# Performance work log

Hardware: AMD Instinct MI355X
Metric: run time of the kernel (lower is better)

The kernel has to match this reference:

```python
import jax, jax.numpy as jnp
import numpy as np
import math

EPS = 1e-5
MAX_NORM = 1.0 - 1e-3
C = 1.0
NUM_HEADS = 8


def _project(x, c=C):
    norm = jnp.maximum(jnp.linalg.norm(x, axis=-1, keepdims=True), EPS)
    max_norm = MAX_NORM / math.sqrt(c)
    return jnp.where(norm > max_norm, x / norm * max_norm, x)


def _expmap0(v, c=C):
    sc = math.sqrt(c)
    n = jnp.maximum(jnp.linalg.norm(v, axis=-1, keepdims=True), EPS)
    return _project(jnp.tanh(sc * n) * v / (sc * n), c)


def _logmap0(y, c=C):
    sc = math.sqrt(c)
    n = jnp.maximum(jnp.linalg.norm(y, axis=-1, keepdims=True), EPS)
    return jnp.arctanh(jnp.minimum(sc * n, 1.0 - EPS)) * y / (sc * n)


def _mobius_add(x, y, c=C):
    x2 = jnp.sum(x * x, axis=-1, keepdims=True)
    y2 = jnp.sum(y * y, axis=-1, keepdims=True)
    xy = jnp.sum(x * y, axis=-1, keepdims=True)
    num = (1.0 + 2.0 * c * xy + c * y2) * x + (1.0 - c * x2) * y
    den = jnp.maximum(1.0 + 2.0 * c * xy + c * c * x2 * y2, EPS)
    return _project(num / den, c)


def _pairwise_dist(x, y, c=C):
    # x: (B,H,Q,d), y: (B,H,K,d) -> (B,H,Q,K)
    m = _mobius_add(-x[:, :, :, None, :], y[:, :, None, :, :], c)  # (B,H,Q,K,d)
    n = jnp.clip(jnp.linalg.norm(m, axis=-1), EPS, 1.0 - EPS)
    sc = math.sqrt(c)
    return (2.0 / sc) * jnp.arctanh(sc * n)


def setup_inputs() -> dict:
    key = jax.random.key(0)
    ks = jax.random.split(key, 12)
    B, S, D = 2, 512, 512
    # points on the Poincare ball via expmap0
    q = _expmap0(0.5 * jax.random.normal(ks[0], (B, S, D), jnp.float32))
    k = _expmap0(0.5 * jax.random.normal(ks[1], (B, S, D), jnp.float32))
    v = _expmap0(0.5 * jax.random.normal(ks[2], (B, S, D), jnp.float32))
    w = 0.02
    return {
        'query': q, 'key': k, 'value': v,
        'Wq': w * jax.random.normal(ks[3], (D, D), jnp.float32),
        'bq': w * jax.random.normal(ks[4], (D,), jnp.float32),
        'Wk': w * jax.random.normal(ks[5], (D, D), jnp.float32),
        'bk': w * jax.random.normal(ks[6], (D,), jnp.float32),
        'Wv': w * jax.random.normal(ks[7], (D, D), jnp.float32),
        'bv': w * jax.random.normal(ks[8], (D,), jnp.float32),
        'Wo': w * jax.random.normal(ks[9], (D, D), jnp.float32),
        'bo': w * jax.random.normal(ks[10], (D,), jnp.float32),
    }


def reference(query, key, value, Wq, bq, Wk, bk, Wv, bv, Wo, bo):
    B, Q, D = query.shape
    K = key.shape[1]
    H = NUM_HEADS
    dh = D // H
    q_tan = _logmap0(query)
    k_tan = _logmap0(key)
    v_tan = _logmap0(value)
    q = (q_tan @ Wq.T + bq).reshape(B, Q, H, dh).transpose(0, 2, 1, 3)  # (B,H,Q,dh)
    k = (k_tan @ Wk.T + bk).reshape(B, K, H, dh).transpose(0, 2, 1, 3)
    v = (v_tan @ Wv.T + bv).reshape(B, K, H, dh).transpose(0, 2, 1, 3)
    q_hyp = _expmap0(q)
    k_hyp = _expmap0(k)
    scores = -_pairwise_dist(q_hyp, k_hyp) / math.sqrt(dh)  # (B,H,Q,K)
    attn = jax.nn.softmax(scores, axis=-1)  # dropout is identity in eval
    out = jnp.einsum('bhqk,bhkd->bhqd', attn, v)
    out = out.transpose(0, 2, 1, 3).reshape(B, Q, D)
    return _expmap0(out @ Wo.T + bo)
```

## Files before the change

### kernel.cpp

```cpp
#include <hip/hip_runtime.h>
#include <cmath>

#define DEV static __device__ __forceinline__

namespace {

constexpr int B = 2, S = 512, D = 512, H = 8;
constexpr int BS = B * S;
constexpr float EPSF = 1e-5f;
constexpr float MAXN = 1.0f - 1e-3f;

typedef unsigned short u16;
typedef unsigned int u32;
typedef __attribute__((ext_vector_type(8))) short bf8_t;
typedef __attribute__((ext_vector_type(8))) _Float16 h8_t;
typedef __attribute__((ext_vector_type(4))) float f4_t;

DEV float waveSum(float v) {
#pragma unroll
  for (int o = 32; o > 0; o >>= 1) v += __shfl_xor(v, o, 64);
  return v;
}
DEV u16 f2bf(float f) {
  u32 x = __float_as_uint(f);
  u32 r = x + 0x7fffu + ((x >> 16) & 1u);
  return (u16)(r >> 16);
}
DEV float bf2f(u16 u) { return __uint_as_float(((u32)u) << 16); }
DEV u16 f2h(float f) {
  _Float16 h = (_Float16)f;
  u16 u;
  __builtin_memcpy(&u, &h, 2);
  return u;
}
DEV float tanh_pos(float n) {
  float e = __builtin_amdgcn_exp2f(2.8853900817779268f * n);
  return (e - 1.f) / (e + 1.f);
}
DEV bf8_t conv8(float4 a, float4 b) {
  bf8_t o;
  o[0] = (short)f2bf(a.x); o[1] = (short)f2bf(a.y);
  o[2] = (short)f2bf(a.z); o[3] = (short)f2bf(a.w);
  o[4] = (short)f2bf(b.x); o[5] = (short)f2bf(b.y);
  o[6] = (short)f2bf(b.z); o[7] = (short)f2bf(b.w);
  return o;
}
DEV float dot4(float4 a) { return a.x * a.x + a.y * a.y + a.z * a.z + a.w * a.w; }

__global__ __launch_bounds__(256) void gemm_qkv_f2(
    const float* __restrict__ q, const float* __restrict__ k,
    const float* __restrict__ v, const float* __restrict__ Wq,
    const float* __restrict__ Wk, const float* __restrict__ Wv,
    const float* __restrict__ bq, const float* __restrict__ bk,
    const float* __restrict__ bv, u16* __restrict__ hq, u16* __restrict__ hk,
    u16* __restrict__ vT, float* __restrict__ qn2, float* __restrict__ kn2) {
  const int z = blockIdx.z;
  const float* A = z == 0 ? q : (z == 1 ? k : v);
  const float* W = z == 0 ? Wq : (z == 1 ? Wk : Wv);
  const float* bias = z == 0 ? bq : (z == 1 ? bk : bv);
  const int i0 = blockIdx.y * 64, j0 = blockIdx.x * 64, h = blockIdx.x;
  __shared__ __align__(16) u16 As[4096], Bs[4096];
  __shared__ float facs[64];
  const int tid = threadIdx.x;
  const int w = tid >> 6, l = tid & 63, lg = l >> 4, lr = l & 15;
  const int srow = tid >> 3, scb = tid & 7;
  f4_t acc[4] = {{0, 0, 0, 0}, {0, 0, 0, 0}, {0, 0, 0, 0}, {0, 0, 0, 0}};
  float n2a = 0.f, n2b = 0.f;
  for (int kt = 0; kt < D; kt += 64) {
    const float* ap0 = A + (size_t)(i0 + srow) * D + kt + scb * 8;
    const float* ap1 = ap0 + (size_t)32 * D;
    const float* wp0 = W + (size_t)(j0 + srow) * D + kt + scb * 8;
    const float* wp1 = wp0 + (size_t)32 * D;
    float4 a00 = *(const float4*)ap0, a01 = *(const float4*)(ap0 + 4);
    float4 a10 = *(const float4*)ap1, a11 = *(const float4*)(ap1 + 4);
    float4 w00 = *(const float4*)wp0, w01 = *(const float4*)(wp0 + 4);
    float4 w10 = *(const float4*)wp1, w11 = *(const float4*)(wp1 + 4);
    n2a += dot4(a00) + dot4(a01);
    n2b += dot4(a10) + dot4(a11);
    __syncthreads();
    const int sw = 8 * (scb ^ (srow & 7));
    *(bf8_t*)&As[srow * 64 + sw] = conv8(a00, a01);
    *(bf8_t*)&As[(srow + 32) * 64 + sw] = conv8(a10, a11);
    *(bf8_t*)&Bs[srow * 64 + sw] = conv8(w00, w01);
    *(bf8_t*)&Bs[(srow + 32) * 64 + sw] = conv8(w10, w11);
    __syncthreads();
#pragma unroll
    for (int ks = 0; ks < 2; ++ks) {
      const int arow = w * 16 + lr;
      bf8_t af = *(const bf8_t*)&As[arow * 64 + 8 * ((ks * 4 + lg) ^ (arow & 7))];
#pragma unroll
      for (int nf = 0; nf < 4; ++nf) {
        const int brow = nf * 16 + lr;
        bf8_t bfr = *(const bf8_t*)&Bs[brow * 64 + 8 * ((ks * 4 + lg) ^ (brow & 7))];
        acc[nf] = __builtin_amdgcn_mfma_f32_16x16x32_bf16(af, bfr, acc[nf], 0, 0, 0);
      }
    }
  }
  n2a += __shfl_xor(n2a, 1, 64); n2a += __shfl_xor(n2a, 2, 64);
  n2a += __shfl_xor(n2a, 4, 64);
  n2b += __shfl_xor(n2b, 1, 64); n2b += __shfl_xor(n2b, 2, 64);
  n2b += __shfl_xor(n2b, 4, 64);
  if (scb == 0) {
    float na = fmaxf(sqrtf(n2a), EPSF), za = fminf(na, 1.0f - EPSF);
    facs[srow] = 0.34657359027997264f *
                 __builtin_amdgcn_logf((1.0f + za) / (1.0f - za)) / na;
    float nb = fmaxf(sqrtf(n2b), EPSF), zb = fminf(nb, 1.0f - EPSF);
    facs[srow + 32] = 0.34657359027997264f *
                      __builtin_amdgcn_logf((1.0f + zb) / (1.0f - zb)) / nb;
  }
  __syncthreads();
  float c[4][4];
#pragma unroll
  for (int nf = 0; nf < 4; ++nf) {
    const float bb = bias[j0 + nf * 16 + lr];
#pragma unroll
    for (int r = 0; r < 4; ++r)
      c[nf][r] = acc[nf][r] * facs[w * 16 + lg * 4 + r] + bb;
  }
  if (z < 2) {
    float part[4] = {0, 0, 0, 0};
#pragma unroll
    for (int nf = 0; nf < 4; ++nf)
#pragma unroll
      for (int r = 0; r < 4; ++r) part[r] += c[nf][r] * c[nf][r];
#pragma unroll
    for (int off = 1; off < 16; off <<= 1)
#pragma unroll
      for (int r = 0; r < 4; ++r) part[r] += __shfl_xor(part[r], off, 64);
    float fac[4];
#pragma unroll
    for (int r = 0; r < 4; ++r) {
      float n = fmaxf(sqrtf(part[r]), EPSF);
      fac[r] = fminf(tanh_pos(n), MAXN) / n;
    }
    u16 yb[4][4];
    float p2[4] = {0, 0, 0, 0};
#pragma unroll
    for (int nf = 0; nf < 4; ++nf)
#pragma unroll
      for (int r = 0; r < 4; ++r) {
        u16 t = f2bf(c[nf][r] * fac[r]);
        yb[nf][r] = t;
        float yf = bf2f(t);
        p2[r] += yf * yf;
      }
#pragma unroll
    for (int off = 1; off < 16; off <<= 1)
#pragma unroll
      for (int r = 0; r < 4; ++r) p2[r] += __shfl_xor(p2[r], off, 64);
    u16* dst = z == 0 ? hq : hk;
    float* n2o = z == 0 ? qn2 : kn2;
#pragma unroll
    for (int nf = 0; nf < 4; ++nf)
#pragma unroll
      for (int r = 0; r < 4; ++r)
        dst[(size_t)(i0 + w * 16 + lg * 4 + r) * D + j0 + nf * 16 + lr] = yb[nf][r];
    if (lr == 0)
#pragma unroll
      for (int r = 0; r < 4; ++r)
        n2o[h * BS + i0 + w * 16 + lg * 4 + r] = p2[r];
  } else {
    __syncthreads();
#pragma unroll
    for (int nf = 0; nf < 4; ++nf)
#pragma unroll
      for (int r = 0; r < 4; ++r) {
        const int prow = w * 16 + lg * 4 + r;
        const int pcol = nf * 16 + lr;
        As[prow * 64 + 8 * ((pcol >> 3) ^ (prow & 7)) + (pcol & 7)] = f2h(c[nf][r]);
      }
    __syncthreads();
    const int d = tid >> 2, s0 = (tid & 3) * 16;
    const int b = i0 >> 9, sb = (i0 & 511) + s0;
    bf8_t o0, o1;
#pragma unroll
    for (int j = 0; j < 8; ++j) {
      const int s = s0 + j;
      o0[j] = (short)As[s * 64 + 8 * ((d >> 3) ^ (s & 7)) + (d & 7)];
    }
#pragma unroll
    for (int j = 0; j < 8; ++j) {
      const int s = s0 + 8 + j;
      o1[j] = (short)As[s * 64 + 8 * ((d >> 3) ^ (s & 7)) + (d & 7)];
    }
    u16* dst = vT + ((size_t)((b * 8 + h) * 64 + d)) * S + sb;
    *(bf8_t*)dst = o0;
    *(bf8_t*)(dst + 8) = o1;
  }
}

__global__ __launch_bounds__(256) void fused_attn_blk(
    const u16* __restrict__ hq, const u16* __restrict__ hk,
    const u16* __restrict__ vT, const float* __restrict__ qn2,
    const float* __restrict__ kn2, u16* __restrict__ ctx) {
  const int bh = blockIdx.y, b = bh >> 3, h = bh & 7;
  const int i0 = blockIdx.x * 16;
  __shared__ __align__(16) u16 Ps[4][2][1024];
  __shared__ float rsL[4][16];
  const int tid = threadIdx.x;
  const int w = tid >> 6, l = tid & 63, lg = l >> 4, lr = l & 15;
  const int sp = w;
  bf8_t qf[2];
#pragma unroll
  for (int ks = 0; ks < 2; ++ks)
    qf[ks] = *(const bf8_t*)(hq + (size_t)(b * S + i0 + lr) * D + h * 64 +
                             ks * 32 + lg * 8);
  float qq[4];
#pragma unroll
  for (int r = 0; r < 4; ++r) qq[r] = qn2[h * BS + b * S + i0 + lg * 4 + r];
  f4_t acc_o[4] = {{0, 0, 0, 0}, {0, 0, 0, 0}, {0, 0, 0, 0}, {0, 0, 0, 0}};
  float rloc[4] = {0, 0, 0, 0};
#pragma unroll
  for (int t = 0; t < 2; ++t) {
    const int kt = sp * 2 + t;
    const int kb = b * S + kt * 64;
    bf8_t kf[2][4], vf[2][4];
#pragma unroll
    for (int ks = 0; ks < 2; ++ks)
#pragma unroll
      for (int nf = 0; nf < 4; ++nf) {
        kf[ks][nf] = *(const bf8_t*)(hk + (size_t)(kb + nf * 16 + lr) * D +
                                     h * 64 + ks * 32 + lg * 8);
        vf[ks][nf] = *(const bf8_t*)(vT + (size_t)(bh * 64 + nf * 16 + lr) * S +
                                     kt * 64 + ks * 32 + lg * 8);
      }
    float kn[4];
#pragma unroll
    for (int nf = 0; nf < 4; ++nf) kn[nf] = kn2[h * BS + kb + nf * 16 + lr];
    f4_t sa[4] = {{0, 0, 0, 0}, {0, 0, 0, 0}, {0, 0, 0, 0}, {0, 0, 0, 0}};
#pragma unroll
    for (int ks = 0; ks < 2; ++ks)
#pragma unroll
      for (int nf = 0; nf < 4; ++nf)
        sa[nf] = __builtin_amdgcn_mfma_f32_16x16x32_bf16(qf[ks], kf[ks][nf],
                                                         sa[nf], 0, 0, 0);
    u16* Pb = Ps[w][t & 1];
    float ps[4] = {0, 0, 0, 0};
#pragma unroll
    for (int nf = 0; nf < 4; ++nf) {
      const float kk = kn[nf];
#pragma unroll
      for (int r = 0; r < 4; ++r) {
        const float tt = sa[nf][r];
        float num = fmaxf(qq[r] - 2.f * tt + kk, 0.f);
        float den = fmaxf(1.f - 2.f * tt + qq[r] * kk, EPSF);
        float rr = fminf(fmaxf(sqrtf(num / den), EPSF), MAXN);
        float p = __builtin_amdgcn_exp2f(
            0.125f * __builtin_amdgcn_logf((1.f - rr) / (1.f + rr)));
        ps[r] += p;
        const int prow = lg * 4 + r, pcol = nf * 16 + lr;
        Pb[prow * 64 + 8 * ((pcol >> 3) ^ (prow & 7)) + (pcol & 7)] = f2h(p);
      }
    }
#pragma unroll
    for (int off = 1; off < 16; off <<= 1)
#pragma unroll
      for (int r = 0; r < 4; ++r) ps[r] += __shfl_xor(ps[r], off, 64);
#pragma unroll
    for (int r = 0; r < 4; ++r) rloc[r] += ps[r];
#pragma unroll
    for (int ks = 0; ks < 2; ++ks) {
      h8_t pa = *(const h8_t*)&Pb[lr * 64 + 8 * ((ks * 4 + lg) ^ (lr & 7))];
#pragma unroll
      for (int nf = 0; nf < 4; ++nf)
        acc_o[nf] = __builtin_amdgcn_mfma_f32_16x16x32_f16(pa, vf[ks][nf],
                                                           acc_o[nf], 0, 0, 0);
    }
  }
  float* myO = (float*)Ps + w * 1024;
#pragma unroll
  for (int nf = 0; nf < 4; ++nf)
#pragma unroll
    for (int r = 0; r < 4; ++r)
      myO[(lg * 4 + r) * 64 + nf * 16 + lr] = acc_o[nf][r];
  if (lr == 0)
#pragma unroll
    for (int r = 0; r < 4; ++r) rsL[w][lg * 4 + r] = rloc[r];
  __syncthreads();
  const float* OsL = (const float*)Ps;
  const int row = tid >> 4, c4 = (tid & 15) * 4;
  const float rt = rsL[0][row] + rsL[1][row] + rsL[2][row] + rsL[3][row];
  const float inv = 1.f / rt;
  f4_t s = {0, 0, 0, 0};
#pragma unroll
  for (int sp2 = 0; sp2 < 4; ++sp2)
    s += *(const f4_t*)&OsL[sp2 * 1024 + row * 64 + c4];
  ushort4 o;
  o.x = f2bf(s[0] * inv); o.y = f2bf(s[1] * inv);
  o.z = f2bf(s[2] * inv); o.w = f2bf(s[3] * inv);
  *(ushort4*)&ctx[(size_t)(b * S + i0 + row) * D + h * 64 + c4] = o;
}

__global__ __launch_bounds__(256) void gemm_out_f(
    const u16* __restrict__ A, const float* __restrict__ Wo,
    const float* __restrict__ bias, float* __restrict__ C) {
  const int i0 = blockIdx.y * 64, j0 = blockIdx.x * 64;
  __shared__ __align__(16) u16 As[4096], Bs[4096];
  const int tid = threadIdx.x;
  const int w = tid >> 6, l = tid & 63, lg = l >> 4, lr = l & 15;
  const int srow = tid >> 3, scb = tid & 7;
  f4_t acc[4] = {{0, 0, 0, 0}, {0, 0, 0, 0}, {0, 0, 0, 0}, {0, 0, 0, 0}};
  for (int kt = 0; kt < D; kt += 64) {
    bf8_t a0 = *(const bf8_t*)(A + (size_t)(i0 + srow) * D + kt + scb * 8);
    bf8_t a1 = *(const bf8_t*)(A + (size_t)(i0 + srow + 32) * D + kt + scb * 8);
    const float* wp0 = Wo + (size_t)(j0 + srow) * D + kt + scb * 8;
    const float* wp1 = wp0 + (size_t)32 * D;
    float4 w00 = *(const float4*)wp0, w01 = *(const float4*)(wp0 + 4);
    float4 w10 = *(const float4*)wp1, w11 = *(const float4*)(wp1 + 4);
    __syncthreads();
    const int sw = 8 * (scb ^ (srow & 7));
    *(bf8_t*)&As[srow * 64 + sw] = a0;
    *(bf8_t*)&As[(srow + 32) * 64 + sw] = a1;
    *(bf8_t*)&Bs[srow * 64 + sw] = conv8(w00, w01);
    *(bf8_t*)&Bs[(srow + 32) * 64 + sw] = conv8(w10, w11);
    __syncthreads();
#pragma unroll
    for (int ks = 0; ks < 2; ++ks) {
      const int arow = w * 16 + lr;
      bf8_t af = *(const bf8_t*)&As[arow * 64 + 8 * ((ks * 4 + lg) ^ (arow & 7))];
#pragma unroll
      for (int nf = 0; nf < 4; ++nf) {
        const int brow = nf * 16 + lr;
        bf8_t bfr = *(const bf8_t*)&Bs[brow * 64 + 8 * ((ks * 4 + lg) ^ (brow & 7))];
        acc[nf] = __builtin_amdgcn_mfma_f32_16x16x32_bf16(af, bfr, acc[nf], 0, 0, 0);
      }
    }
  }
#pragma unroll
  for (int nf = 0; nf < 4; ++nf) {
    const int j = j0 + nf * 16 + lr;
    const float bb = bias[j];
#pragma unroll
    for (int r = 0; r < 4; ++r)
      C[(size_t)(i0 + w * 16 + lg * 4 + r) * D + j] = acc[nf][r] + bb;
  }
}

__global__ __launch_bounds__(256) void expmap_rows_full(
    const float* __restrict__ in, float* __restrict__ out) {
  const int row = blockIdx.x;
  const float2 xv = *(const float2*)(in + (size_t)row * D + threadIdx.x * 2);
  float s = xv.x * xv.x + xv.y * xv.y;
  __shared__ float sh[4];
  float ws = waveSum(s);
  if ((threadIdx.x & 63) == 0) sh[threadIdx.x >> 6] = ws;
  __syncthreads();
  float tot = sh[0] + sh[1] + sh[2] + sh[3];
  float n = fmaxf(sqrtf(tot), EPSF);
  float fac = fminf(tanh_pos(n), MAXN) / n;
  float2 o = make_float2(xv.x * fac, xv.y * fac);
  *(float2*)(out + (size_t)row * D + threadIdx.x * 2) = o;
}

}

extern "C" void kernel_launch(void* const* d_in, const int* in_sizes, int n_in,
                              void* d_out, int out_size, void* d_ws,
                              size_t ws_size, hipStream_t stream) {
  const float* q = (const float*)d_in[0];
  const float* k = (const float*)d_in[1];
  const float* v = (const float*)d_in[2];
  const float* Wq = (const float*)d_in[3];
  const float* bq = (const float*)d_in[4];
  const float* Wk = (const float*)d_in[5];
  const float* bk = (const float*)d_in[6];
  const float* Wv = (const float*)d_in[7];
  const float* bv = (const float*)d_in[8];
  const float* Wo = (const float*)d_in[9];
  const float* bo = (const float*)d_in[10];
  float* out = (float*)d_out;

  char* w8 = (char*)d_ws;
  u16* hq = (u16*)(w8 + 0);
  u16* hk = (u16*)(w8 + 1048576);
  u16* vT = (u16*)(w8 + 2097152);
  float* qn2 = (float*)(w8 + 3145728);
  float* kn2 = (float*)(w8 + 3178496);
  u16* ctx = (u16*)(w8 + 3211264);
  float* olin = (float*)(w8 + 4259840);

  gemm_qkv_f2<<<dim3(8, 16, 3), 256, 0, stream>>>(q, k, v, Wq, Wk, Wv, bq, bk,
                                                  bv, hq, hk, vT, qn2, kn2);
  fused_attn_blk<<<dim3(32, 16), 256, 0, stream>>>(hq, hk, vT, qn2, kn2, ctx);
  gemm_out_f<<<dim3(8, 16), 256, 0, stream>>>(ctx, Wo, bo, olin);
  expmap_rows_full<<<dim3(BS), 256, 0, stream>>>(olin, out);
}
```

Before: 41.83 us.

## Pre-convert Wo to bf16 in QKV kernel and shrink output GEMM tiles

The z==2 blocks of the QKV projection kernel now also convert the Wo weight matrix from fp32 to bf16 into a workspace buffer. The output GEMM reads these bf16 weights directly instead of loading fp32 and converting each tile, which halves its weight traffic and removes repeated conversion. The output GEMM tile is also cut from 64x64 to 32x64, doubling the grid to 256 blocks for better CU occupancy. The cost is extra global writes during the first kernel and a larger workspace footprint.

```diff
diff --git a/kernel.cpp b/kernel.cpp
--- a/kernel.cpp
+++ b/kernel.cpp
@@ -51,9 +51,11 @@
     const float* __restrict__ q, const float* __restrict__ k,
     const float* __restrict__ v, const float* __restrict__ Wq,
     const float* __restrict__ Wk, const float* __restrict__ Wv,
-    const float* __restrict__ bq, const float* __restrict__ bk,
-    const float* __restrict__ bv, u16* __restrict__ hq, u16* __restrict__ hk,
-    u16* __restrict__ vT, float* __restrict__ qn2, float* __restrict__ kn2) {
+    const float* __restrict__ Wo, const float* __restrict__ bq,
+    const float* __restrict__ bk, const float* __restrict__ bv,
+    u16* __restrict__ hq, u16* __restrict__ hk, u16* __restrict__ vT,
+    float* __restrict__ qn2, float* __restrict__ kn2,
+    u16* __restrict__ wobf) {
   const int z = blockIdx.z;
   const float* A = z == 0 ? q : (z == 1 ? k : v);
   const float* W = z == 0 ? Wq : (z == 1 ? Wk : Wv);
@@ -64,6 +66,13 @@
   const int tid = threadIdx.x;
   const int w = tid >> 6, l = tid & 63, lg = l >> 4, lr = l & 15;
   const int srow = tid >> 3, scb = tid & 7;
+  if (z == 2) {
+    const int bid = blockIdx.y * 8 + blockIdx.x;
+    const int off = bid * 2048 + tid * 8;
+    float4 wa = *(const float4*)(Wo + off);
+    float4 wb = *(const float4*)(Wo + off + 4);
+    *(bf8_t*)(wobf + off) = conv8(wa, wb);
+  }
   f4_t acc[4] = {{0, 0, 0, 0}, {0, 0, 0, 0}, {0, 0, 0, 0}, {0, 0, 0, 0}};
   float n2a = 0.f, n2b = 0.f;
   for (int kt = 0; kt < D; kt += 64) {
@@ -291,48 +300,45 @@
   *(ushort4*)&ctx[(size_t)(b * S + i0 + row) * D + h * 64 + c4] = o;
 }
 
-__global__ __launch_bounds__(256) void gemm_out_f(
-    const u16* __restrict__ A, const float* __restrict__ Wo,
+__global__ __launch_bounds__(256) void gemm_out_b(
+    const u16* __restrict__ A, const u16* __restrict__ Wob,
     const float* __restrict__ bias, float* __restrict__ C) {
-  const int i0 = blockIdx.y * 64, j0 = blockIdx.x * 64;
-  __shared__ __align__(16) u16 As[4096], Bs[4096];
+  const int i0 = blockIdx.y * 32, j0 = blockIdx.x * 64;
+  __shared__ __align__(16) u16 As[2048], Bs[4096];
   const int tid = threadIdx.x;
   const int w = tid >> 6, l = tid & 63, lg = l >> 4, lr = l & 15;
   const int srow = tid >> 3, scb = tid & 7;
-  f4_t acc[4] = {{0, 0, 0, 0}, {0, 0, 0, 0}, {0, 0, 0, 0}, {0, 0, 0, 0}};
+  const int mrow = (w >> 1) * 16, ncol = (w & 1) * 32;
+  f4_t acc[2] = {{0, 0, 0, 0}, {0, 0, 0, 0}};
   for (int kt = 0; kt < D; kt += 64) {
     bf8_t a0 = *(const bf8_t*)(A + (size_t)(i0 + srow) * D + kt + scb * 8);
-    bf8_t a1 = *(const bf8_t*)(A + (size_t)(i0 + srow + 32) * D + kt + scb * 8);
-    const float* wp0 = Wo + (size_t)(j0 + srow) * D + kt + scb * 8;
-    const float* wp1 = wp0 + (size_t)32 * D;
-    float4 w00 = *(const float4*)wp0, w01 = *(const float4*)(wp0 + 4);
-    float4 w10 = *(const float4*)wp1, w11 = *(const float4*)(wp1 + 4);
+    bf8_t w0 = *(const bf8_t*)(Wob + (size_t)(j0 + srow) * D + kt + scb * 8);
+    bf8_t w1 = *(const bf8_t*)(Wob + (size_t)(j0 + srow + 32) * D + kt + scb * 8);
     __syncthreads();
     const int sw = 8 * (scb ^ (srow & 7));
     *(bf8_t*)&As[srow * 64 + sw] = a0;
-    *(bf8_t*)&As[(srow + 32) * 64 + sw] = a1;
-    *(bf8_t*)&Bs[srow * 64 + sw] = conv8(w00, w01);
-    *(bf8_t*)&Bs[(srow + 32) * 64 + sw] = conv8(w10, w11);
+    *(bf8_t*)&Bs[srow * 64 + sw] = w0;
+    *(bf8_t*)&Bs[(srow + 32) * 64 + sw] = w1;
     __syncthreads();
 #pragma unroll
     for (int ks = 0; ks < 2; ++ks) {
-      const int arow = w * 16 + lr;
+      const int arow = mrow + lr;
       bf8_t af = *(const bf8_t*)&As[arow * 64 + 8 * ((ks * 4 + lg) ^ (arow & 7))];
 #pragma unroll
-      for (int nf = 0; nf < 4; ++nf) {
-        const int brow = nf * 16 + lr;
+      for (int nf = 0; nf < 2; ++nf) {
+        const int brow = ncol + nf * 16 + lr;
         bf8_t bfr = *(const bf8_t*)&Bs[brow * 64 + 8 * ((ks * 4 + lg) ^ (brow & 7))];
         acc[nf] = __builtin_amdgcn_mfma_f32_16x16x32_bf16(af, bfr, acc[nf], 0, 0, 0);
       }
     }
   }
 #pragma unroll
-  for (int nf = 0; nf < 4; ++nf) {
-    const int j = j0 + nf * 16 + lr;
+  for (int nf = 0; nf < 2; ++nf) {
+    const int j = j0 + ncol + nf * 16 + lr;
     const float bb = bias[j];
 #pragma unroll
     for (int r = 0; r < 4; ++r)
-      C[(size_t)(i0 + w * 16 + lg * 4 + r) * D + j] = acc[nf][r] + bb;
+      C[(size_t)(i0 + mrow + lg * 4 + r) * D + j] = acc[nf][r] + bb;
   }
 }
 
@@ -378,10 +384,12 @@
   float* kn2 = (float*)(w8 + 3178496);
   u16* ctx = (u16*)(w8 + 3211264);
   float* olin = (float*)(w8 + 4259840);
-
-  gemm_qkv_f2<<<dim3(8, 16, 3), 256, 0, stream>>>(q, k, v, Wq, Wk, Wv, bq, bk,
-                                                  bv, hq, hk, vT, qn2, kn2);
+  u16* wobf = (u16*)(w8 + 6357000 + 504);
+  wobf = (u16*)(w8 + 6357504);
+
+  gemm_qkv_f2<<<dim3(8, 16, 3), 256, 0, stream>>>(
+      q, k, v, Wq, Wk, Wv, Wo, bq, bk, bv, hq, hk, vT, qn2, kn2, wobf);
   fused_attn_blk<<<dim3(32, 16), 256, 0, stream>>>(hq, hk, vT, qn2, kn2, ctx);
-  gemm_out_f<<<dim3(8, 16), 256, 0, stream>>>(ctx, Wo, bo, olin);
+  gemm_out_b<<<dim3(8, 32), 256, 0, stream>>>(ctx, wobf, bo, olin);
   expmap_rows_full<<<dim3(BS), 256, 0, stream>>>(olin, out);
 }
```

Result: faster. 39.03 us (-6.7%).
